# Kernel optimization log

Hardware: AMD Instinct MI355X
Metric: run time of the kernel (lower is better)

Reference implementation:

```python
import jax, jax.numpy as jnp
import numpy as np

NUM_HEADS = 16
LAMBDA = 0.1
HADAMARD_SCALE = 0.05
ROPE_BASE = 10000.0


def _rope(t):
    # t: [B, H, S, hd] -- rotary embedding (half-split convention)
    hd = t.shape[-1]
    S = t.shape[2]
    half = hd // 2
    inv_freq = 1.0 / (ROPE_BASE ** (jnp.arange(half, dtype=jnp.float32) / half))
    ang = jnp.arange(S, dtype=jnp.float32)[:, None] * inv_freq[None, :]  # [S, half]
    cos = jnp.cos(ang).astype(t.dtype)
    sin = jnp.sin(ang).astype(t.dtype)
    t1, t2 = t[..., :half], t[..., half:]
    return jnp.concatenate([t1 * cos - t2 * sin, t2 * cos + t1 * sin], axis=-1)


def _rotate_half(t):
    half = t.shape[-1] // 2
    return jnp.concatenate([-t[..., half:], t[..., :half]], axis=-1)


def setup_inputs() -> dict:
    key = jax.random.key(0)
    ks = jax.random.split(key, 6)
    B, S, D = 2, 2048, 1024
    scale = 1.0 / np.sqrt(D).astype(np.float32)
    x = jax.random.normal(ks[0], (B, S, D), jnp.float32)
    Wq = jax.random.normal(ks[1], (D, D), jnp.float32) * scale
    Wk = jax.random.normal(ks[2], (D, D), jnp.float32) * scale
    Wv = jax.random.normal(ks[3], (D, D), jnp.float32) * scale
    Wo = jax.random.normal(ks[4], (D, D), jnp.float32) * scale
    gate_w = jax.random.normal(ks[5], (D // NUM_HEADS,), jnp.float32) * 0.01
    return {"x": x, "Wq": Wq, "Wk": Wk, "Wv": Wv, "Wo": Wo, "gate_w": gate_w}


def reference(x, Wq, Wk, Wv, Wo, gate_w):
    B, S, D = x.shape
    H = NUM_HEADS
    hd = D // H

    def heads(W):
        return (x @ W.T).reshape(B, S, H, hd).transpose(0, 2, 1, 3)  # [B,H,S,hd]

    Q = _rope(heads(Wq))
    K = _rope(heads(Wk))
    V = heads(Wv)

    causal = jnp.tril(jnp.ones((S, S), dtype=bool))
    inv_sqrt_d = 1.0 / jnp.sqrt(jnp.asarray(hd, x.dtype))

    def attend(q, k):
        # first-order + lambda * second-order (elementwise-squared) scores
        s = (jnp.einsum('bhsd,bhtd->bhst', q, k)
             + LAMBDA * jnp.einsum('bhsd,bhtd->bhst', q * q, k * k)) * inv_sqrt_d
        s = jnp.where(causal, s, jnp.asarray(-1e9, s.dtype))
        a = jax.nn.softmax(s, axis=-1)
        return jnp.einsum('bhst,bhtd->bhsd', a, V)

    out1 = attend(Q, K)                                  # standard pass
    out2 = attend(_rotate_half(Q), _rotate_half(K))      # rotated second pass

    # hadamard gate mix of the two passes
    out = 0.5 * (out1 + out2) + HADAMARD_SCALE * (out1 * out2) * gate_w

    out = out.transpose(0, 2, 1, 3).reshape(B, S, D)
    return out @ Wo.T
```

## Files before the change

### kernel.cpp

```cpp
#include <hip/hip_runtime.h>

typedef unsigned short u16;
typedef __attribute__((ext_vector_type(4))) unsigned short u16x4;
typedef __attribute__((ext_vector_type(8))) unsigned short u16x8;
typedef __attribute__((ext_vector_type(8))) short s16x8;
typedef __attribute__((ext_vector_type(4))) float f32x4;

__device__ __forceinline__ u16 f2bf(float f) {
  unsigned int u = __float_as_uint(f);
  u += 0x7FFFu + ((u >> 16) & 1u);
  return (u16)(u >> 16);
}
__device__ __forceinline__ float bf2f(u16 h) {
  return __uint_as_float(((unsigned int)h) << 16);
}

__device__ __forceinline__ void gload_lds16(const u16* g, u16* l) {
  __builtin_amdgcn_global_load_lds(
      (const __attribute__((address_space(1))) unsigned int*)(g),
      (__attribute__((address_space(3))) unsigned int*)(l), 16, 0, 0);
}

__global__ __launch_bounds__(256) void cvt_kernel(const float* __restrict__ src,
                                                  u16* __restrict__ dst, int n4) {
  int i = blockIdx.x * 256 + threadIdx.x;
  if (i >= n4) return;
  float4 v = reinterpret_cast<const float4*>(src)[i];
  u16x4 o;
  o.x = f2bf(v.x); o.y = f2bf(v.y); o.z = f2bf(v.z); o.w = f2bf(v.w);
  reinterpret_cast<u16x4*>(dst)[i] = o;
}

__global__ __launch_bounds__(256) void cvt_w(const float* __restrict__ Wq,
                                             const float* __restrict__ Wk,
                                             const float* __restrict__ Wv,
                                             const float* __restrict__ Wo,
                                             u16* __restrict__ wbf, u16* __restrict__ wobf) {
  int blk = blockIdx.x;
  int sel = blk >> 10;
  const float* src = (sel == 0) ? Wq : (sel == 1) ? Wk : (sel == 2) ? Wv : Wo;
  u16* dst = (sel < 3) ? (wbf + (size_t)sel * 1048576) : wobf;
  int i = (blk & 1023) * 256 + threadIdx.x;
  float4 v = reinterpret_cast<const float4*>(src)[i];
  u16x4 o;
  o.x = f2bf(v.x); o.y = f2bf(v.y); o.z = f2bf(v.z); o.w = f2bf(v.w);
  reinterpret_cast<u16x4*>(dst)[i] = o;
}

__device__ __forceinline__ void store_out(float* p, float v) { *p = v; }
__device__ __forceinline__ void store_out(u16* p, float v) { *p = f2bf(v); }

template <typename OutT>
__global__ __launch_bounds__(256) void gemm_bt(const u16* __restrict__ A,
                                               const u16* __restrict__ Bw,
                                               OutT* __restrict__ C, int N, int K) {
  __shared__ u16 As[4096];
  __shared__ u16 Bs[4096];
  const int tid = threadIdx.x;
  const int lane = tid & 63;
  const int wave = tid >> 6;
  const int wm = wave >> 1, wn = wave & 1;
  const int lh = lane & 15, quad = lane >> 4;
  const int q8 = quad * 8;
  const int m0 = blockIdx.y * 128, n0 = blockIdx.x * 128;

  f32x4 acc[4][4];
#pragma unroll
  for (int i = 0; i < 4; ++i)
#pragma unroll
    for (int j = 0; j < 4; ++j) { acc[i][j][0] = 0.f; acc[i][j][1] = 0.f; acc[i][j][2] = 0.f; acc[i][j][3] = 0.f; }

  const int nkt = K >> 5;
  for (int kt = 0; kt < nkt; ++kt) {
    const int kb = kt * 32;
    __syncthreads();
#pragma unroll
    for (int i = 0; i < 4; ++i) {
      const int c = wave * 4 + i;
      if (c < 8) {
        gload_lds16(A + (size_t)(m0 + c * 16 + lh) * K + kb + q8, &As[c * 512 + lane * 8]);
      } else {
        const int rb = c - 8;
        gload_lds16(Bw + (size_t)(n0 + rb * 16 + lh) * K + kb + q8, &Bs[rb * 512 + lane * 8]);
      }
    }
    __syncthreads();
    s16x8 af[4], bf4[4];
#pragma unroll
    for (int mb = 0; mb < 4; ++mb)
      af[mb] = *reinterpret_cast<const s16x8*>(&As[(wm * 4 + mb) * 512 + lane * 8]);
#pragma unroll
    for (int nb = 0; nb < 4; ++nb)
      bf4[nb] = *reinterpret_cast<const s16x8*>(&Bs[(wn * 4 + nb) * 512 + lane * 8]);
#pragma unroll
    for (int mb = 0; mb < 4; ++mb)
#pragma unroll
      for (int nb = 0; nb < 4; ++nb)
        acc[mb][nb] = __builtin_amdgcn_mfma_f32_16x16x32_bf16(af[mb], bf4[nb], acc[mb][nb], 0, 0, 0);
  }
#pragma unroll
  for (int mb = 0; mb < 4; ++mb)
#pragma unroll
    for (int nb = 0; nb < 4; ++nb) {
      const int col = n0 + wn * 64 + nb * 16 + lh;
#pragma unroll
      for (int r = 0; r < 4; ++r) {
        const int row = m0 + wm * 64 + mb * 16 + quad * 4 + r;
        store_out(&C[(size_t)row * N + col], acc[mb][nb][r]);
      }
    }
}

__global__ __launch_bounds__(256) void rope_kernel(const u16* __restrict__ raw,
                                                   u16* __restrict__ Qs, u16* __restrict__ Q2s,
                                                   u16* __restrict__ Kb, u16* __restrict__ K2b) {
  int idx = blockIdx.x * 256 + threadIdx.x;
  int which = idx >> 21;
  int id = idx & 0x1FFFFF;
  int d = id & 31;
  int s = (id >> 5) & 2047;
  int bh = id >> 16;
  int b = bh >> 4;
  int h = bh & 15;
  const u16* r = raw + (size_t)(b * 2048 + s) * 3072 + which * 1024 + h * 64 + d;
  float v1 = bf2f(r[0]);
  float v2 = bf2f(r[32]);
  float invf = __expf((float)d * -0.2878231366f);
  float ang = (float)s * invf;
  float sv, cv;
  __sincosf(ang, &sv, &cv);
  float e0 = v1 * cv - v2 * sv;
  float e1 = v2 * cv + v1 * sv;
  size_t ofs = (size_t)(bh * 2048 + s) * 64 + d;
  if (which == 0) {
    Qs[ofs]       = f2bf(e0 * 0.125f);
    Qs[ofs + 32]  = f2bf(e1 * 0.125f);
    Q2s[ofs]      = f2bf(e0 * e0 * 0.0125f);
    Q2s[ofs + 32] = f2bf(e1 * e1 * 0.0125f);
  } else {
    Kb[ofs]       = f2bf(e0);
    Kb[ofs + 32]  = f2bf(e1);
    K2b[ofs]      = f2bf(e0 * e0);
    K2b[ofs + 32] = f2bf(e1 * e1);
  }
}

__global__ __launch_bounds__(256) void transpose_v(const u16* __restrict__ raw,
                                                   u16* __restrict__ Vt) {
  int st = blockIdx.x, bh = blockIdx.y;
  int b = bh >> 4, h = bh & 15;
  __shared__ u16 tile[64 * 72];
  int tid = threadIdx.x;
#pragma unroll
  for (int it = 0; it < 4; ++it) {
    int c = it * 256 + tid;
    int sr = c >> 4, d4 = c & 15;
    u16x4 v = *reinterpret_cast<const u16x4*>(
        raw + (size_t)(b * 2048 + st * 64 + sr) * 3072 + 2048 + h * 64 + d4 * 4);
    *reinterpret_cast<u16x4*>(&tile[sr * 72 + d4 * 4]) = v;
  }
  __syncthreads();
#pragma unroll
  for (int it = 0; it < 4; ++it) {
    int c = it * 256 + tid;
    int dd = c >> 4, s4 = c & 15;
    u16x4 v;
#pragma unroll
    for (int j = 0; j < 4; ++j) v[j] = tile[(s4 * 4 + j) * 72 + dd];
    *reinterpret_cast<u16x4*>(Vt + (size_t)(bh * 64 + dd) * 2048 + st * 64 + s4 * 4) = v;
  }
}

__global__ __launch_bounds__(256, 2) void attn_kernel(const u16* __restrict__ Qs,
                                                      const u16* __restrict__ Q2s,
                                                      const u16* __restrict__ Kb,
                                                      const u16* __restrict__ K2b,
                                                      const u16* __restrict__ Vt,
                                                      const float* __restrict__ gate,
                                                      u16* __restrict__ attn,
                                                      float* __restrict__ Opart,
                                                      float* __restrict__ Lpart) {
  const int bx = blockIdx.x;
  const int g = bx / 3, t = bx - 3 * g;
  int qi, kt0, kt1, half;
  bool split;
  if (t < 2) { qi = 15 - g; split = true;  half = t; const int nk = qi + 1; kt0 = t * nk; kt1 = kt0 + nk - 1; }
  else       { qi = 7 - g;  split = false; half = 0; kt0 = 0; kt1 = 2 * qi + 1; }
  const int bh = blockIdx.y;
  const int tid = threadIdx.x, lane = tid & 63, wave = tid >> 6;
  const int lh = lane & 15, quad = lane >> 4;
  const int b = bh >> 4, h = bh & 15;
  __shared__ u16 stageS[2][8192];
  __shared__ u16 Pbuf[4][2][1152];
  const int base = qi * 128 + wave * 32;
  const int q8 = quad * 8;

  auto do_stage = [&](int buf, int kt) {
#pragma unroll
    for (int i = 0; i < 4; ++i) {
      const int c = wave * 4 + i;
      const int t2 = c >> 3, f = c & 7, kk = f >> 2, nb = f & 3;
      const u16* src = (t2 ? K2b : Kb) +
          (size_t)(bh * 2048 + kt * 64 + nb * 16 + lh) * 64 + kk * 32 + q8;
      gload_lds16(src, &stageS[buf][t2 * 4096 + f * 512 + lane * 8]);
    }
  };

  s16x8 qf[2][2], q2f[2][2];
#pragma unroll
  for (int mb = 0; mb < 2; ++mb) {
    const size_t qoff = (size_t)(bh * 2048 + base + mb * 16 + lh) * 64 + q8;
#pragma unroll
    for (int kk = 0; kk < 2; ++kk) {
      qf[mb][kk]  = *reinterpret_cast<const s16x8*>(Qs + qoff + kk * 32);
      q2f[mb][kk] = *reinterpret_cast<const s16x8*>(Q2s + qoff + kk * 32);
    }
  }

  f32x4 oacc[2][4];
  float lsum[2][4];
#pragma unroll
  for (int mb = 0; mb < 2; ++mb)
#pragma unroll
    for (int nb = 0; nb < 4; ++nb) { oacc[mb][nb][0] = 0.f; oacc[mb][nb][1] = 0.f; oacc[mb][nb][2] = 0.f; oacc[mb][nb][3] = 0.f; }
#pragma unroll
  for (int mb = 0; mb < 2; ++mb)
#pragma unroll
    for (int r = 0; r < 4; ++r) lsum[mb][r] = 0.f;
  float gw[4];
#pragma unroll
  for (int nb = 0; nb < 4; ++nb) gw[nb] = gate[nb * 16 + lh];

  do_stage(0, kt0);
  __syncthreads();

  const int wmaxrow = base + 31;
  for (int kt = kt0; kt <= kt1; ++kt) {
    const int p = (kt - kt0) & 1;
    if (kt < kt1) do_stage(1 - p, kt + 1);

    if (kt * 64 <= wmaxrow) {
      const u16* Ks = stageS[p];
      f32x4 sacc[2][4];
#pragma unroll
      for (int mb = 0; mb < 2; ++mb)
#pragma unroll
        for (int nb = 0; nb < 4; ++nb) { sacc[mb][nb][0] = -8.f; sacc[mb][nb][1] = -8.f; sacc[mb][nb][2] = -8.f; sacc[mb][nb][3] = -8.f; }
#pragma unroll
      for (int nb = 0; nb < 4; ++nb)
#pragma unroll
        for (int kk = 0; kk < 2; ++kk) {
          s16x8 kf  = *reinterpret_cast<const s16x8*>(&Ks[(kk * 4 + nb) * 512 + lane * 8]);
          s16x8 k2f = *reinterpret_cast<const s16x8*>(&Ks[4096 + (kk * 4 + nb) * 512 + lane * 8]);
#pragma unroll
          for (int mb = 0; mb < 2; ++mb) {
            sacc[mb][nb] = __builtin_amdgcn_mfma_f32_16x16x32_bf16(qf[mb][kk],  kf,  sacc[mb][nb], 0, 0, 0);
            sacc[mb][nb] = __builtin_amdgcn_mfma_f32_16x16x32_bf16(q2f[mb][kk], k2f, sacc[mb][nb], 0, 0, 0);
          }
        }
      s16x8 vf[2][4];
#pragma unroll
      for (int kk = 0; kk < 2; ++kk)
#pragma unroll
        for (int nb = 0; nb < 4; ++nb)
          vf[kk][nb] = *reinterpret_cast<const s16x8*>(
              Vt + (size_t)(bh * 64 + nb * 16 + lh) * 2048 + kt * 64 + kk * 32 + q8);

      if (kt * 64 + 63 > base) {
#pragma unroll
        for (int mb = 0; mb < 2; ++mb)
#pragma unroll
          for (int nb = 0; nb < 4; ++nb) {
            const int colg = kt * 64 + nb * 16 + lh;
#pragma unroll
            for (int r = 0; r < 4; ++r) {
              const int rowg = base + mb * 16 + quad * 4 + r;
              if (colg > rowg) sacc[mb][nb][r] = -1e9f;
            }
          }
      }
#pragma unroll
      for (int mb = 0; mb < 2; ++mb)
#pragma unroll
        for (int nb = 0; nb < 4; ++nb)
#pragma unroll
          for (int r = 0; r < 4; ++r) {
            float pv = __expf(sacc[mb][nb][r]);
            lsum[mb][r] += pv;
            Pbuf[wave][mb][(quad * 4 + r) * 72 + nb * 16 + lh] = f2bf(pv);
          }
#pragma unroll
      for (int mb = 0; mb < 2; ++mb)
#pragma unroll
        for (int kk = 0; kk < 2; ++kk) {
          s16x8 pf = *reinterpret_cast<const s16x8*>(&Pbuf[wave][mb][lh * 72 + kk * 32 + q8]);
#pragma unroll
          for (int nb = 0; nb < 4; ++nb)
            oacc[mb][nb] = __builtin_amdgcn_mfma_f32_16x16x32_bf16(pf, vf[kk][nb], oacc[mb][nb], 0, 0, 0);
        }
    }
    __syncthreads();
  }
#pragma unroll
  for (int mb = 0; mb < 2; ++mb)
#pragma unroll
    for (int r = 0; r < 4; ++r) {
      float rs = lsum[mb][r];
#pragma unroll
      for (int off = 1; off < 16; off <<= 1) rs += __shfl_xor(rs, off);
      lsum[mb][r] = rs;
    }
  if (split) {
#pragma unroll
    for (int mb = 0; mb < 2; ++mb)
#pragma unroll
      for (int r = 0; r < 4; ++r) {
        const int rowRel = base + mb * 16 + quad * 4 + r - 1024;
        const size_t orow = ((size_t)half * 32768 + bh * 1024 + rowRel);
        if (lh == 0) Lpart[orow] = lsum[mb][r];
#pragma unroll
        for (int nb = 0; nb < 4; ++nb)
          Opart[orow * 64 + nb * 16 + lh] = oacc[mb][nb][r];
      }
  } else {
#pragma unroll
    for (int mb = 0; mb < 2; ++mb)
#pragma unroll
      for (int r = 0; r < 4; ++r) {
        const float invl = 1.0f / lsum[mb][r];
        const int rows = base + mb * 16 + quad * 4 + r;
#pragma unroll
        for (int nb = 0; nb < 4; ++nb) {
          float o = oacc[mb][nb][r] * invl;
          float val = o + 0.05f * o * o * gw[nb];
          attn[(size_t)(b * 2048 + rows) * 1024 + h * 64 + nb * 16 + lh] = f2bf(val);
        }
      }
  }
}

__global__ __launch_bounds__(256) void combine_kernel(const float* __restrict__ Opart,
                                                      const float* __restrict__ Lpart,
                                                      const float* __restrict__ gate,
                                                      u16* __restrict__ attn) {
  int idx = blockIdx.x * 256 + threadIdx.x;
  int d = idx & 63;
  int rowi = idx >> 6;
  int bh = rowi >> 10, rr = rowi & 1023;
  float o = Opart[idx] + Opart[idx + 2097152];
  float l = Lpart[rowi] + Lpart[rowi + 32768];
  o /= l;
  float val = o + 0.05f * o * o * gate[d];
  int b = bh >> 4, h = bh & 15;
  int s = 1024 + rr;
  attn[(size_t)(b * 2048 + s) * 1024 + h * 64 + d] = f2bf(val);
}

extern "C" void kernel_launch(void* const* d_in, const int* in_sizes, int n_in,
                              void* d_out, int out_size, void* d_ws, size_t ws_size,
                              hipStream_t stream) {
  (void)in_sizes; (void)n_in; (void)out_size; (void)ws_size;
  const float* x    = (const float*)d_in[0];
  const float* Wq   = (const float*)d_in[1];
  const float* Wk   = (const float*)d_in[2];
  const float* Wv   = (const float*)d_in[3];
  const float* Wo   = (const float*)d_in[4];
  const float* gate = (const float*)d_in[5];

  u16* ws    = (u16*)d_ws;
  u16* xbf   = ws;
  u16* wbf   = xbf + 4194304;
  u16* wobf  = wbf + 3145728;
  u16* raw   = wobf + 1048576;
  u16* Qsb   = raw + 12582912;
  u16* Kbb   = Qsb + 4194304;
  u16* K2bb  = Kbb + 4194304;
  u16* Vtb   = K2bb + 4194304;
  float* Opart = (float*)(Vtb + 4194304);
  float* Lpart = Opart + 4194304;
  u16* Q2sb  = xbf;
  u16* attnb = raw;

  cvt_kernel<<<4096, 256, 0, stream>>>(x, xbf, 1048576);
  cvt_w<<<4096, 256, 0, stream>>>(Wq, Wk, Wv, Wo, wbf, wobf);

  gemm_bt<u16><<<dim3(24, 32), 256, 0, stream>>>(xbf, wbf, raw, 3072, 1024);
  rope_kernel<<<16384, 256, 0, stream>>>(raw, Qsb, Q2sb, Kbb, K2bb);
  transpose_v<<<dim3(32, 32), 256, 0, stream>>>(raw, Vtb);
  attn_kernel<<<dim3(24, 32), 256, 0, stream>>>(Qsb, Q2sb, Kbb, K2bb, Vtb, gate, attnb,
                                                Opart, Lpart);
  combine_kernel<<<8192, 256, 0, stream>>>(Opart, Lpart, gate, attnb);
  gemm_bt<float><<<dim3(8, 32), 256, 0, stream>>>(attnb, wobf, (float*)d_out, 1024, 1024);
}
```

Measured before the change: 268.3 us.

## Drop LDS K staging, raise attention occupancy, and split more query blocks

```diff
diff --git a/kernel.cpp b/kernel.cpp
--- a/kernel.cpp
+++ b/kernel.cpp
@@ -171,7 +171,7 @@
   }
 }
 
-__global__ __launch_bounds__(256, 2) void attn_kernel(const u16* __restrict__ Qs,
+__global__ __launch_bounds__(256, 4) void attn_kernel(const u16* __restrict__ Qs,
                                                       const u16* __restrict__ Q2s,
                                                       const u16* __restrict__ Kb,
                                                       const u16* __restrict__ K2b,
@@ -179,32 +179,29 @@
                                                       const float* __restrict__ gate,
                                                       u16* __restrict__ attn,
                                                       float* __restrict__ Opart,
-                                                      float* __restrict__ Lpart) {
+                                                      float* __restrict__ Lpart,
+                                                      float* __restrict__ Opart2,
+                                                      float* __restrict__ Lpart2) {
   const int bx = blockIdx.x;
-  const int g = bx / 3, t = bx - 3 * g;
-  int qi, kt0, kt1, half;
+  int qi, kt0, kt1, half, which;
   bool split;
-  if (t < 2) { qi = 15 - g; split = true;  half = t; const int nk = qi + 1; kt0 = t * nk; kt1 = kt0 + nk - 1; }
-  else       { qi = 7 - g;  split = false; half = 0; kt0 = 0; kt1 = 2 * qi + 1; }
+  if (bx < 16) {
+    qi = 15 - (bx >> 1); half = bx & 1; split = true; which = 0;
+    const int nk = qi + 1; kt0 = half * nk; kt1 = kt0 + nk - 1;
+  } else if (bx < 24) {
+    const int t = bx - 16;
+    qi = 7 - (t >> 1); half = t & 1; split = true; which = 1;
+    const int nk = qi + 1; kt0 = half * nk; kt1 = kt0 + nk - 1;
+  } else {
+    qi = 27 - bx; split = false; which = 0; half = 0; kt0 = 0; kt1 = 2 * qi + 1;
+  }
   const int bh = blockIdx.y;
   const int tid = threadIdx.x, lane = tid & 63, wave = tid >> 6;
   const int lh = lane & 15, quad = lane >> 4;
   const int b = bh >> 4, h = bh & 15;
-  __shared__ u16 stageS[2][8192];
   __shared__ u16 Pbuf[4][2][1152];
   const int base = qi * 128 + wave * 32;
   const int q8 = quad * 8;
-
-  auto do_stage = [&](int buf, int kt) {
-#pragma unroll
-    for (int i = 0; i < 4; ++i) {
-      const int c = wave * 4 + i;
-      const int t2 = c >> 3, f = c & 7, kk = f >> 2, nb = f & 3;
-      const u16* src = (t2 ? K2b : Kb) +
-          (size_t)(bh * 2048 + kt * 64 + nb * 16 + lh) * 64 + kk * 32 + q8;
-      gload_lds16(src, &stageS[buf][t2 * 4096 + f * 512 + lane * 8]);
-    }
-  };
 
   s16x8 qf[2][2], q2f[2][2];
 #pragma unroll
@@ -217,6 +214,10 @@
     }
   }
 
+  const u16* kfp  = Kb  + (size_t)(bh * 2048 + lh) * 64 + q8;
+  const u16* k2fp = K2b + (size_t)(bh * 2048 + lh) * 64 + q8;
+  const u16* vfp  = Vt  + (size_t)(bh * 64 + lh) * 2048 + q8;
+
   f32x4 oacc[2][4];
   float lsum[2][4];
 #pragma unroll
@@ -231,75 +232,66 @@
 #pragma unroll
   for (int nb = 0; nb < 4; ++nb) gw[nb] = gate[nb * 16 + lh];
 
-  do_stage(0, kt0);
-  __syncthreads();
-
   const int wmaxrow = base + 31;
   for (int kt = kt0; kt <= kt1; ++kt) {
-    const int p = (kt - kt0) & 1;
-    if (kt < kt1) do_stage(1 - p, kt + 1);
-
-    if (kt * 64 <= wmaxrow) {
-      const u16* Ks = stageS[p];
-      f32x4 sacc[2][4];
+    if (kt * 64 > wmaxrow) continue;
+
+    f32x4 sacc[2][4];
+#pragma unroll
+    for (int mb = 0; mb < 2; ++mb)
+#pragma unroll
+      for (int nb = 0; nb < 4; ++nb) { sacc[mb][nb][0] = -8.f; sacc[mb][nb][1] = -8.f; sacc[mb][nb][2] = -8.f; sacc[mb][nb][3] = -8.f; }
+#pragma unroll
+    for (int nb = 0; nb < 4; ++nb)
+#pragma unroll
+      for (int kk = 0; kk < 2; ++kk) {
+        s16x8 kf  = *reinterpret_cast<const s16x8*>(kfp  + kt * 4096 + nb * 1024 + kk * 32);
+        s16x8 k2f = *reinterpret_cast<const s16x8*>(k2fp + kt * 4096 + nb * 1024 + kk * 32);
+#pragma unroll
+        for (int mb = 0; mb < 2; ++mb) {
+          sacc[mb][nb] = __builtin_amdgcn_mfma_f32_16x16x32_bf16(qf[mb][kk],  kf,  sacc[mb][nb], 0, 0, 0);
+          sacc[mb][nb] = __builtin_amdgcn_mfma_f32_16x16x32_bf16(q2f[mb][kk], k2f, sacc[mb][nb], 0, 0, 0);
+        }
+      }
+    s16x8 vf[2][4];
+#pragma unroll
+    for (int kk = 0; kk < 2; ++kk)
+#pragma unroll
+      for (int nb = 0; nb < 4; ++nb)
+        vf[kk][nb] = *reinterpret_cast<const s16x8*>(vfp + (size_t)nb * 32768 + kt * 64 + kk * 32);
+
+    if (kt * 64 + 63 > base) {
 #pragma unroll
       for (int mb = 0; mb < 2; ++mb)
 #pragma unroll
-        for (int nb = 0; nb < 4; ++nb) { sacc[mb][nb][0] = -8.f; sacc[mb][nb][1] = -8.f; sacc[mb][nb][2] = -8.f; sacc[mb][nb][3] = -8.f; }
-#pragma unroll
-      for (int nb = 0; nb < 4; ++nb)
-#pragma unroll
-        for (int kk = 0; kk < 2; ++kk) {
-          s16x8 kf  = *reinterpret_cast<const s16x8*>(&Ks[(kk * 4 + nb) * 512 + lane * 8]);
-          s16x8 k2f = *reinterpret_cast<const s16x8*>(&Ks[4096 + (kk * 4 + nb) * 512 + lane * 8]);
-#pragma unroll
-          for (int mb = 0; mb < 2; ++mb) {
-            sacc[mb][nb] = __builtin_amdgcn_mfma_f32_16x16x32_bf16(qf[mb][kk],  kf,  sacc[mb][nb], 0, 0, 0);
-            sacc[mb][nb] = __builtin_amdgcn_mfma_f32_16x16x32_bf16(q2f[mb][kk], k2f, sacc[mb][nb], 0, 0, 0);
+        for (int nb = 0; nb < 4; ++nb) {
+          const int colg = kt * 64 + nb * 16 + lh;
+#pragma unroll
+          for (int r = 0; r < 4; ++r) {
+            const int rowg = base + mb * 16 + quad * 4 + r;
+            if (colg > rowg) sacc[mb][nb][r] = -1e9f;
           }
         }
-      s16x8 vf[2][4];
-#pragma unroll
-      for (int kk = 0; kk < 2; ++kk)
+    }
+#pragma unroll
+    for (int mb = 0; mb < 2; ++mb)
+#pragma unroll
+      for (int nb = 0; nb < 4; ++nb)
+#pragma unroll
+        for (int r = 0; r < 4; ++r) {
+          float pv = __expf(sacc[mb][nb][r]);
+          lsum[mb][r] += pv;
+          Pbuf[wave][mb][(quad * 4 + r) * 72 + nb * 16 + lh] = f2bf(pv);
+        }
+#pragma unroll
+    for (int mb = 0; mb < 2; ++mb)
+#pragma unroll
+      for (int kk = 0; kk < 2; ++kk) {
+        s16x8 pf = *reinterpret_cast<const s16x8*>(&Pbuf[wave][mb][lh * 72 + kk * 32 + q8]);
 #pragma unroll
         for (int nb = 0; nb < 4; ++nb)
-          vf[kk][nb] = *reinterpret_cast<const s16x8*>(
-              Vt + (size_t)(bh * 64 + nb * 16 + lh) * 2048 + kt * 64 + kk * 32 + q8);
-
-      if (kt * 64 + 63 > base) {
-#pragma unroll
-        for (int mb = 0; mb < 2; ++mb)
-#pragma unroll
-          for (int nb = 0; nb < 4; ++nb) {
-            const int colg = kt * 64 + nb * 16 + lh;
-#pragma unroll
-            for (int r = 0; r < 4; ++r) {
-              const int rowg = base + mb * 16 + quad * 4 + r;
-              if (colg > rowg) sacc[mb][nb][r] = -1e9f;
-            }
-          }
-      }
-#pragma unroll
-      for (int mb = 0; mb < 2; ++mb)
-#pragma unroll
-        for (int nb = 0; nb < 4; ++nb)
-#pragma unroll
-          for (int r = 0; r < 4; ++r) {
-            float pv = __expf(sacc[mb][nb][r]);
-            lsum[mb][r] += pv;
-            Pbuf[wave][mb][(quad * 4 + r) * 72 + nb * 16 + lh] = f2bf(pv);
-          }
-#pragma unroll
-      for (int mb = 0; mb < 2; ++mb)
-#pragma unroll
-        for (int kk = 0; kk < 2; ++kk) {
-          s16x8 pf = *reinterpret_cast<const s16x8*>(&Pbuf[wave][mb][lh * 72 + kk * 32 + q8]);
-#pragma unroll
-          for (int nb = 0; nb < 4; ++nb)
-            oacc[mb][nb] = __builtin_amdgcn_mfma_f32_16x16x32_bf16(pf, vf[kk][nb], oacc[mb][nb], 0, 0, 0);
-        }
-    }
-    __syncthreads();
+          oacc[mb][nb] = __builtin_amdgcn_mfma_f32_16x16x32_bf16(pf, vf[kk][nb], oacc[mb][nb], 0, 0, 0);
+      }
   }
 #pragma unroll
   for (int mb = 0; mb < 2; ++mb)
@@ -315,12 +307,20 @@
     for (int mb = 0; mb < 2; ++mb)
 #pragma unroll
       for (int r = 0; r < 4; ++r) {
-        const int rowRel = base + mb * 16 + quad * 4 + r - 1024;
-        const size_t orow = ((size_t)half * 32768 + bh * 1024 + rowRel);
-        if (lh == 0) Lpart[orow] = lsum[mb][r];
-#pragma unroll
-        for (int nb = 0; nb < 4; ++nb)
-          Opart[orow * 64 + nb * 16 + lh] = oacc[mb][nb][r];
+        const int rowg = base + mb * 16 + quad * 4 + r;
+        if (which == 0) {
+          const size_t orow = (size_t)half * 32768 + bh * 1024 + (rowg - 1024);
+          if (lh == 0) Lpart[orow] = lsum[mb][r];
+#pragma unroll
+          for (int nb = 0; nb < 4; ++nb)
+            Opart[orow * 64 + nb * 16 + lh] = oacc[mb][nb][r];
+        } else {
+          const size_t orow = (size_t)half * 16384 + bh * 512 + (rowg - 512);
+          if (lh == 0) Lpart2[orow] = lsum[mb][r];
+#pragma unroll
+          for (int nb = 0; nb < 4; ++nb)
+            Opart2[orow * 64 + nb * 16 + lh] = oacc[mb][nb][r];
+        }
       }
   } else {
 #pragma unroll
@@ -341,18 +341,29 @@
 
 __global__ __launch_bounds__(256) void combine_kernel(const float* __restrict__ Opart,
                                                       const float* __restrict__ Lpart,
+                                                      const float* __restrict__ Opart2,
+                                                      const float* __restrict__ Lpart2,
                                                       const float* __restrict__ gate,
                                                       u16* __restrict__ attn) {
   int idx = blockIdx.x * 256 + threadIdx.x;
   int d = idx & 63;
-  int rowi = idx >> 6;
-  int bh = rowi >> 10, rr = rowi & 1023;
-  float o = Opart[idx] + Opart[idx + 2097152];
-  float l = Lpart[rowi] + Lpart[rowi + 32768];
+  int r_all = idx >> 6;
+  float o, l;
+  int bh, s;
+  if (r_all < 32768) {
+    o = Opart[idx] + Opart[idx + 2097152];
+    l = Lpart[r_all] + Lpart[r_all + 32768];
+    bh = r_all >> 10; s = 1024 + (r_all & 1023);
+  } else {
+    const int r2 = r_all - 32768;
+    const int i2 = idx - 2097152;
+    o = Opart2[i2] + Opart2[i2 + 1048576];
+    l = Lpart2[r2] + Lpart2[r2 + 16384];
+    bh = r2 >> 9; s = 512 + (r2 & 511);
+  }
   o /= l;
   float val = o + 0.05f * o * o * gate[d];
   int b = bh >> 4, h = bh & 15;
-  int s = 1024 + rr;
   attn[(size_t)(b * 2048 + s) * 1024 + h * 64 + d] = f2bf(val);
 }
 
@@ -380,6 +391,8 @@
   float* Lpart = Opart + 4194304;
   u16* Q2sb  = xbf;
   u16* attnb = raw;
+  float* Opart2 = (float*)(raw + 4194304);
+  float* Lpart2 = Opart2 + 2097152;
 
   cvt_kernel<<<4096, 256, 0, stream>>>(x, xbf, 1048576);
   cvt_w<<<4096, 256, 0, stream>>>(Wq, Wk, Wv, Wo, wbf, wobf);
@@ -387,8 +400,8 @@
   gemm_bt<u16><<<dim3(24, 32), 256, 0, stream>>>(xbf, wbf, raw, 3072, 1024);
   rope_kernel<<<16384, 256, 0, stream>>>(raw, Qsb, Q2sb, Kbb, K2bb);
   transpose_v<<<dim3(32, 32), 256, 0, stream>>>(raw, Vtb);
-  attn_kernel<<<dim3(24, 32), 256, 0, stream>>>(Qsb, Q2sb, Kbb, K2bb, Vtb, gate, attnb,
-                                                Opart, Lpart);
-  combine_kernel<<<8192, 256, 0, stream>>>(Opart, Lpart, gate, attnb);
+  attn_kernel<<<dim3(28, 32), 256, 0, stream>>>(Qsb, Q2sb, Kbb, K2bb, Vtb, gate, attnb,
+                                                Opart, Lpart, Opart2, Lpart2);
+  combine_kernel<<<12288, 256, 0, stream>>>(Opart, Lpart, Opart2, Lpart2, gate, attnb);
   gemm_bt<float><<<dim3(8, 32), 256, 0, stream>>>(attnb, wobf, (float*)d_out, 1024, 1024);
 }
```

Measured after the change: 398.9 us. +48.7%, slower.
